# Performance work log

Hardware: AMD Instinct MI355X
Metric: run time of the kernel (lower is better)

The kernel has to match this reference:

```python
import jax, jax.numpy as jnp
import numpy as np

N = 100000
E = 1600000
D_IN = 64
D_HID = 64


def setup_inputs() -> dict:
    key = jax.random.key(0)
    k1, k2, k3 = jax.random.split(key, 3)
    x = jax.random.normal(k1, (N, D_IN), dtype=jnp.float32)
    edge_index = jax.random.randint(k2, (2, E), 0, N, dtype=jnp.int64)
    # GCNConv linear weight (Glorot-like scale) and bias (zeros at init)
    W = jax.random.normal(k3, (D_IN, D_HID), dtype=jnp.float32) * (1.0 / np.sqrt(D_IN))
    b = jnp.zeros((D_HID,), dtype=jnp.float32)
    return {"x": x, "edge_index": edge_index, "W": W, "b": b}


def gcn_conv(x, edge_index, W, b):
    n = x.shape[0]
    # dense projection first (PyG GCNConv applies lin before propagate)
    xw = x @ W  # [N, D_HID]
    # add self-loops
    loop = jnp.arange(n, dtype=edge_index.dtype)
    src = jnp.concatenate([edge_index[0], loop])  # [E + N]
    dst = jnp.concatenate([edge_index[1], loop])
    # symmetric degree normalization with self-loops, unit edge weights
    ones = jnp.ones(src.shape[0], dtype=xw.dtype)
    deg = jax.ops.segment_sum(ones, dst, num_segments=n)  # [N]
    dinv = jnp.where(deg > 0, jax.lax.rsqrt(deg), 0.0)
    norm = dinv[src] * dinv[dst]  # [E + N]
    # gather, scale, scatter-add
    msgs = xw[src] * norm[:, None]  # [E + N, D_HID]
    out = jax.ops.segment_sum(msgs, dst, num_segments=n)  # [N, D_HID]
    return out + b


def reference(x, edge_index, W, b):
    return gcn_conv(x, edge_index, W, b)
```

## Files before the change

kernel.cpp:

```cpp
#include <hip/hip_runtime.h>
#include <hip/hip_fp16.h>

#define NN 100000
#define NE 1600000
#define D 64
#define SPAN 512
#define NB 196
#define BCAP 10240
#define ECH 4096
#define NP1 ((NE + ECH - 1) / ECH)
#define RB 128
#define NXB ((NN + RB - 1) / RB)

__global__ void k_part(const int* __restrict__ src, const int* __restrict__ dst,
                       int* __restrict__ bcur, unsigned* __restrict__ brecs, int e) {
    __shared__ int hist[256];
    __shared__ int excl[256];
    __shared__ int cur[256];
    __shared__ int gbase[256];
    __shared__ unsigned stage[ECH];
    __shared__ unsigned char stgb[ECH];

    int tid = threadIdx.x;
    int e0  = blockIdx.x * ECH;
    int ecnt = min(ECH, e - e0);

    hist[tid] = 0;
    __syncthreads();

    for (int i = tid * 4; i < ecnt; i += 1024) {
        if (i + 3 < ecnt) {
            int4 d = *(const int4*)(dst + e0 + i);
            atomicAdd(&hist[d.x >> 9], 1);
            atomicAdd(&hist[d.y >> 9], 1);
            atomicAdd(&hist[d.z >> 9], 1);
            atomicAdd(&hist[d.w >> 9], 1);
        } else {
            for (int j = i; j < ecnt; ++j) atomicAdd(&hist[dst[e0 + j] >> 9], 1);
        }
    }
    __syncthreads();

    int v = hist[tid];
    excl[tid] = v;
    __syncthreads();
    for (int off = 1; off < 256; off <<= 1) {
        int t = (tid >= off) ? excl[tid - off] : 0;
        __syncthreads();
        excl[tid] += t;
        __syncthreads();
    }
    int ex = excl[tid] - v;
    __syncthreads();
    excl[tid] = ex;
    cur[tid]  = ex;
    if (v > 0) gbase[tid] = atomicAdd(&bcur[tid], v);
    __syncthreads();

    for (int i = tid * 4; i < ecnt; i += 1024) {
        if (i + 3 < ecnt) {
            int4 d = *(const int4*)(dst + e0 + i);
            int4 s = *(const int4*)(src + e0 + i);
            int bk; int p;
            bk = d.x >> 9; p = atomicAdd(&cur[bk], 1); stage[p] = ((unsigned)s.x << 9) | (unsigned)(d.x & 511); stgb[p] = (unsigned char)bk;
            bk = d.y >> 9; p = atomicAdd(&cur[bk], 1); stage[p] = ((unsigned)s.y << 9) | (unsigned)(d.y & 511); stgb[p] = (unsigned char)bk;
            bk = d.z >> 9; p = atomicAdd(&cur[bk], 1); stage[p] = ((unsigned)s.z << 9) | (unsigned)(d.z & 511); stgb[p] = (unsigned char)bk;
            bk = d.w >> 9; p = atomicAdd(&cur[bk], 1); stage[p] = ((unsigned)s.w << 9) | (unsigned)(d.w & 511); stgb[p] = (unsigned char)bk;
        } else {
            for (int j = i; j < ecnt; ++j) {
                int dd = dst[e0 + j], ss = src[e0 + j];
                int bk = dd >> 9;
                int p = atomicAdd(&cur[bk], 1);
                stage[p] = ((unsigned)ss << 9) | (unsigned)(dd & 511);
                stgb[p] = (unsigned char)bk;
            }
        }
    }
    __syncthreads();

    for (int i = tid; i < ecnt; i += 256) {
        unsigned rec = stage[i];
        int bk = stgb[i];
        int gp = gbase[bk] + (i - excl[bk]);
        if (gp < BCAP)
            brecs[(size_t)bk * BCAP + gp] = rec;
    }
}

__global__ void __launch_bounds__(512)
k_fine(const unsigned* __restrict__ brecs, const int* __restrict__ bcur,
       int* __restrict__ cnt, int* __restrict__ rowstart,
       int* __restrict__ recs2, int n) {
    __shared__ int lcnt[SPAN];
    __shared__ int lcur[SPAN];
    __shared__ int tmp[512];
    __shared__ int sh_bbase;

    int b   = blockIdx.x;
    int tid = threadIdx.x;

    lcnt[tid] = 0;

    tmp[tid] = (tid < NB) ? min(bcur[tid], BCAP) : 0;
    __syncthreads();
    for (int off = 1; off < 512; off <<= 1) {
        int u = (tid >= off) ? tmp[tid - off] : 0;
        __syncthreads();
        tmp[tid] += u;
        __syncthreads();
    }
    if (tid == 0) sh_bbase = (b == 0) ? 0 : tmp[b - 1];

    int nrec = min(bcur[b], BCAP);
    const unsigned* rb = brecs + (size_t)b * BCAP;

    for (int i = tid; i < nrec; i += 512)
        atomicAdd(&lcnt[rb[i] & 511], 1);
    __syncthreads();

    int v = lcnt[tid];
    tmp[tid] = v;
    __syncthreads();
    for (int off = 1; off < 512; off <<= 1) {
        int u = (tid >= off) ? tmp[tid - off] : 0;
        __syncthreads();
        tmp[tid] += u;
        __syncthreads();
    }
    int ex = tmp[tid] - v;
    lcur[tid] = ex;
    __syncthreads();

    int base = sh_bbase;
    int node = b * SPAN + tid;
    if (node < n) {
        cnt[node] = v;
        rowstart[node] = base + ex;
    }

    for (int i = tid; i < nrec; i += 512) {
        unsigned rec = rb[i];
        int dl = rec & 511;
        int p = atomicAdd(&lcur[dl], 1);
        recs2[base + p] = (int)(rec >> 9);
    }
}

__global__ void __launch_bounds__(128)
k_xw2h(const float* __restrict__ x, const float* __restrict__ W,
       const int* __restrict__ cnt, __half* __restrict__ xw2, int n) {
    __shared__ float sW[D][68];
    __shared__ float sx[RB][64];

    int tid = threadIdx.x;
    int w   = tid >> 6;
    int l   = tid & 63;
    int rg  = l >> 3;
    int cg  = l & 7;
    int rowbase = blockIdx.x * RB;

#pragma unroll
    for (int i = 0; i < 8; ++i) {
        int f = i * 128 + tid;
        int k = f >> 4, c4 = (f & 15) * 4;
        *(float4*)(&sW[k][c4]) = *(const float4*)(W + k * D + c4);
    }
#pragma unroll
    for (int i = 0; i < 16; ++i) {
        int f = i * 128 + tid;
        int row = f >> 4, kc = f & 15;
        int gr = rowbase + row; if (gr >= n) gr = n - 1;
        float4 v = *(const float4*)(x + (size_t)gr * D + kc * 4);
        int sc = kc ^ ((row >> 3) & 7);
        *(float4*)(&sx[row][sc * 4]) = v;
    }
    __syncthreads();

    int rb0 = w * 64 + rg * 8;
    float acc[8][8];
#pragma unroll
    for (int rr = 0; rr < 8; ++rr)
#pragma unroll
        for (int cc = 0; cc < 8; ++cc) acc[rr][cc] = 0.f;

    int swz = (rb0 >> 3) & 7;
    for (int ks = 0; ks < 16; ++ks) {
        float4 xv[8];
#pragma unroll
        for (int rr = 0; rr < 8; ++rr)
            xv[rr] = *(const float4*)(&sx[rb0 + rr][(ks ^ swz) * 4]);
#pragma unroll
        for (int j = 0; j < 4; ++j) {
            int k = ks * 4 + j;
            float4 w0 = *(const float4*)(&sW[k][cg * 8]);
            float4 w1 = *(const float4*)(&sW[k][cg * 8 + 4]);
#pragma unroll
            for (int rr = 0; rr < 8; ++rr) {
                float xs = (j == 0) ? xv[rr].x : (j == 1) ? xv[rr].y : (j == 2) ? xv[rr].z : xv[rr].w;
                acc[rr][0] += xs * w0.x;
                acc[rr][1] += xs * w0.y;
                acc[rr][2] += xs * w0.z;
                acc[rr][3] += xs * w0.w;
                acc[rr][4] += xs * w1.x;
                acc[rr][5] += xs * w1.y;
                acc[rr][6] += xs * w1.z;
                acc[rr][7] += xs * w1.w;
            }
        }
    }

    union H2U { __half2 h; unsigned u; };
#pragma unroll
    for (int rr = 0; rr < 8; ++rr) {
        int grow = rowbase + rb0 + rr;
        if (grow >= n) break;
        float di = rsqrtf((float)cnt[grow] + 1.0f);
        int4 pk;
        H2U a, bb, c, d;
        a.h  = __half2(__float2half_rn(acc[rr][0] * di), __float2half_rn(acc[rr][1] * di));
        bb.h = __half2(__float2half_rn(acc[rr][2] * di), __float2half_rn(acc[rr][3] * di));
        c.h  = __half2(__float2half_rn(acc[rr][4] * di), __float2half_rn(acc[rr][5] * di));
        d.h  = __half2(__float2half_rn(acc[rr][6] * di), __float2half_rn(acc[rr][7] * di));
        pk.x = (int)a.u; pk.y = (int)bb.u; pk.z = (int)c.u; pk.w = (int)d.u;
        *(int4*)(xw2 + (size_t)grow * D + cg * 8) = pk;
    }
}

__global__ void k_gather(const int* __restrict__ recs, const int* __restrict__ rowstart,
                         const int* __restrict__ cnt, const __half* __restrict__ xw2,
                         const float* __restrict__ b, float* __restrict__ out, int n) {
    int wid  = (blockIdx.x * blockDim.x + threadIdx.x) >> 6;
    int lane = threadIdx.x & 63;
    if (wid >= n) return;

    int base = __builtin_amdgcn_readfirstlane(rowstart[wid]);
    int k    = __builtin_amdgcn_readfirstlane(cnt[wid]);

    float acc = __half2float(xw2[(size_t)wid * D + lane]);

    int i = 0;
    for (; i + 4 <= k; i += 4) {
        int s0 = recs[base + i + 0];
        int s1 = recs[base + i + 1];
        int s2 = recs[base + i + 2];
        int s3 = recs[base + i + 3];
        float v0 = __half2float(xw2[(size_t)s0 * D + lane]);
        float v1 = __half2float(xw2[(size_t)s1 * D + lane]);
        float v2 = __half2float(xw2[(size_t)s2 * D + lane]);
        float v3 = __half2float(xw2[(size_t)s3 * D + lane]);
        acc += (v0 + v1) + (v2 + v3);
    }
    for (; i < k; ++i)
        acc += __half2float(xw2[(size_t)recs[base + i] * D + lane]);

    float di = rsqrtf((float)k + 1.0f);
    out[(size_t)wid * D + lane] = acc * di + b[lane];
}

extern "C" void kernel_launch(void* const* d_in, const int* in_sizes, int n_in,
                              void* d_out, int out_size, void* d_ws, size_t ws_size,
                              hipStream_t stream) {
    const float* x  = (const float*)d_in[0];
    const int*   ei = (const int*)d_in[1];
    const float* W  = (const float*)d_in[2];
    const float* b  = (const float*)d_in[3];
    float* out = (float*)d_out;

    __half*   xw2      = (__half*)d_ws;
    int*      cnt      = (int*)(xw2 + (size_t)NN * D);
    int*      rowstart = cnt + NN;
    int*      bcur     = rowstart + NN;
    unsigned* brecs    = (unsigned*)(bcur + NB);
    int*      recs2    = (int*)(brecs + (size_t)NB * BCAP);

    const int* src = ei;
    const int* dst = ei + NE;

    hipMemsetAsync(bcur, 0, NB * sizeof(int), stream);

    k_part <<<NP1, 256, 0, stream>>>(src, dst, bcur, brecs, NE);
    k_fine <<<NB, 512, 0, stream>>>(brecs, bcur, cnt, rowstart, recs2, NN);
    k_xw2h <<<NXB, 128, 0, stream>>>(x, W, cnt, xw2, NN);

    long long tot = (long long)NN * 64;
    k_gather<<<(int)((tot + 255) / 256), 256, 0, stream>>>(recs2, rowstart, cnt, xw2, b, out, NN);
}
```

Before: 115.5 us.

## Gather eight neighbor rows per wavefront with 16-byte loads and shuffle reduction

The gather kernel now splits each 64-lane wavefront into 8 edge groups of 8 lanes. Each lane loads 8 fp16 features with one int4 load, so a wavefront processes 8 neighbors per iteration instead of one row per step with 2-byte loads. Partial sums are combined with xor shuffles, and 8 lanes write the output as float4 stores. This is meant to cut load instruction count and raise memory-level parallelism, at the cost of the shuffle reduction and of idle lanes when the degree is not a multiple of 8.

```diff
diff --git a/kernel.cpp b/kernel.cpp
--- a/kernel.cpp
+++ b/kernel.cpp
@@ -230,31 +230,63 @@
                          const int* __restrict__ cnt, const __half* __restrict__ xw2,
                          const float* __restrict__ b, float* __restrict__ out, int n) {
     int wid  = (blockIdx.x * blockDim.x + threadIdx.x) >> 6;
+    if (wid >= n) return;
     int lane = threadIdx.x & 63;
-    if (wid >= n) return;
+    int eg   = lane >> 3;
+    int cb   = lane & 7;
 
     int base = __builtin_amdgcn_readfirstlane(rowstart[wid]);
     int k    = __builtin_amdgcn_readfirstlane(cnt[wid]);
 
-    float acc = __half2float(xw2[(size_t)wid * D + lane]);
-
-    int i = 0;
-    for (; i + 4 <= k; i += 4) {
-        int s0 = recs[base + i + 0];
-        int s1 = recs[base + i + 1];
-        int s2 = recs[base + i + 2];
-        int s3 = recs[base + i + 3];
-        float v0 = __half2float(xw2[(size_t)s0 * D + lane]);
-        float v1 = __half2float(xw2[(size_t)s1 * D + lane]);
-        float v2 = __half2float(xw2[(size_t)s2 * D + lane]);
-        float v3 = __half2float(xw2[(size_t)s3 * D + lane]);
-        acc += (v0 + v1) + (v2 + v3);
-    }
-    for (; i < k; ++i)
-        acc += __half2float(xw2[(size_t)recs[base + i] * D + lane]);
-
-    float di = rsqrtf((float)k + 1.0f);
-    out[(size_t)wid * D + lane] = acc * di + b[lane];
+    float acc[8];
+#pragma unroll
+    for (int j = 0; j < 8; ++j) acc[j] = 0.f;
+
+    for (int i0 = 0; i0 < k; i0 += 8) {
+        int e = i0 + eg;
+        if (e < k) {
+            int s = recs[base + e];
+            int4 v = *((const int4*)(xw2 + (size_t)s * D) + cb);
+            const __half2* hp = (const __half2*)&v;
+            float2 f0 = __half22float2(hp[0]);
+            float2 f1 = __half22float2(hp[1]);
+            float2 f2 = __half22float2(hp[2]);
+            float2 f3 = __half22float2(hp[3]);
+            acc[0] += f0.x; acc[1] += f0.y;
+            acc[2] += f1.x; acc[3] += f1.y;
+            acc[4] += f2.x; acc[5] += f2.y;
+            acc[6] += f3.x; acc[7] += f3.y;
+        }
+    }
+
+#pragma unroll
+    for (int m = 8; m < 64; m <<= 1)
+#pragma unroll
+        for (int j = 0; j < 8; ++j)
+            acc[j] += __shfl_xor(acc[j], m, 64);
+
+    if (eg == 0) {
+        float di = rsqrtf((float)k + 1.0f);
+        int4 sv = *((const int4*)(xw2 + (size_t)wid * D) + cb);
+        const __half2* sp = (const __half2*)&sv;
+        float2 s0 = __half22float2(sp[0]);
+        float2 s1 = __half22float2(sp[1]);
+        float2 s2 = __half22float2(sp[2]);
+        float2 s3 = __half22float2(sp[3]);
+        float4 b0 = *(const float4*)(b + cb * 8);
+        float4 b1 = *(const float4*)(b + cb * 8 + 4);
+        float4 o0, o1;
+        o0.x = (acc[0] + s0.x) * di + b0.x;
+        o0.y = (acc[1] + s0.y) * di + b0.y;
+        o0.z = (acc[2] + s1.x) * di + b0.z;
+        o0.w = (acc[3] + s1.y) * di + b0.w;
+        o1.x = (acc[4] + s2.x) * di + b1.x;
+        o1.y = (acc[5] + s2.y) * di + b1.y;
+        o1.z = (acc[6] + s3.x) * di + b1.z;
+        o1.w = (acc[7] + s3.y) * di + b1.w;
+        *(float4*)(out + (size_t)wid * D + cb * 8)     = o0;
+        *(float4*)(out + (size_t)wid * D + cb * 8 + 4) = o1;
+    }
 }
 
 extern "C" void kernel_launch(void* const* d_in, const int* in_sizes, int n_in,
```

After: 114.9 us. About the same (-0.5%).
